# Kernel tuning notes

Measured on AMD Instinct MI355X. Metric: run time of the kernel, lower is better.

Reference implementation:

```python
import jax, jax.numpy as jnp
import numpy as np

BINS = 32
NUM_ACTION = 12


def _conv(x, w, b, stride, pad):
    y = jax.lax.conv_general_dilated(x, w, (stride, stride), [(pad, pad), (pad, pad)],
                                     dimension_numbers=('NCHW', 'OIHW', 'NCHW'))
    return y + b[None, :, None, None]


def _maxpool3s2(x):
    return jax.lax.reduce_window(x, -jnp.inf, jax.lax.max, (1, 1, 3, 3), (1, 1, 2, 2), 'VALID')


def _area_resize(x, oh, ow):
    b, c, h, w = x.shape  # exact area interp when h%oh==0, w%ow==0
    return x.reshape(b, c, oh, h // oh, ow, w // ow).mean(axis=(3, 5))


def _sobel_mag(gray):
    # kornia.filters.Sobel: normalized sobel kernels (abs-sum=1), replicate pad, sqrt(gx^2+gy^2+eps)
    kx = jnp.array([[-1., 0., 1.], [-2., 0., 2.], [-1., 0., 1.]], jnp.float32) / 8.0
    k = jnp.stack([kx, kx.T])[:, None]  # [2,1,3,3]
    p = jnp.pad(gray, ((0, 0), (0, 0), (1, 1), (1, 1)), mode='edge')
    g = jax.lax.conv_general_dilated(p, k, (1, 1), 'VALID',
                                     dimension_numbers=('NCHW', 'OIHW', 'NCHW'))
    return jnp.sqrt(jnp.sum(g * g, axis=1, keepdims=True) + 1e-6)


def _hist_feature(img):
    # Fused replacement for FeatureExtractor's python triple-loop of torch.histc calls.
    # img: [B,1,H,W] with values in [0,1]. Scale 0: whole-image hist; scale 1: the 4
    # quadrants of the full-res image; third bins-slot stays zero (loop only runs 2 scales).
    b, _, h, w = img.shape
    idx = jnp.clip((img[:, 0] * BINS).astype(jnp.int32), 0, BINS - 1)  # [B,H,W]
    hist = lambda i: jnp.zeros((BINS,), jnp.float32).at[i.ravel()].add(1.0)
    h0 = jax.vmap(hist)(idx) / (h * w)                                  # [B,BINS]
    h2, w2 = h // 2, w // 2
    blocks = idx.reshape(b, 2, h2, 2, w2).transpose(0, 1, 3, 2, 4).reshape(b * 4, h2 * w2)
    h1 = jax.vmap(hist)(blocks).reshape(b, 2, 2, BINS) / (h2 * w2)      # [B,2,2,BINS]
    out0 = jnp.broadcast_to(h0[:, :, None, None], (b, BINS, 4, 4))
    out1 = jnp.repeat(jnp.repeat(h1.transpose(0, 3, 1, 2), 2, axis=2), 2, axis=3)
    out2 = jnp.zeros_like(out0)
    return jnp.concatenate([out0, out1, out2], axis=1)                  # [B,3*BINS,4,4]


def _l2norm(x):
    return x / (jnp.linalg.norm(x, axis=1, keepdims=True) + 1e-7)


def _forward(image, w1, b1, w2, b2, w3, b3, w4, b4, w5, b5, fc1_w, fc1_b, fc2_w, fc2_b):
    b = image.shape[0]
    rgb = jnp.stack([image[:, 0], 0.5 * (image[:, 1] + image[:, 2]), image[:, 3]], axis=1)
    # AlexNet conv backbone on area-resized 112x112 -> [B,256,2,2]
    x = _area_resize(rgb, 112, 112)
    x = _maxpool3s2(jax.nn.relu(_conv(x, w1, b1, 4, 2)))
    x = _maxpool3s2(jax.nn.relu(_conv(x, w2, b2, 1, 2)))
    x = jax.nn.relu(_conv(x, w3, b3, 1, 1))
    x = jax.nn.relu(_conv(x, w4, b4, 1, 1))
    x = _maxpool3s2(jax.nn.relu(_conv(x, w5, b5, 1, 1)))
    f_sem = x.reshape(b, -1)                                            # [B,1024]
    gray = (0.299 * rgb[:, 0] + 0.587 * rgb[:, 1] + 0.114 * rgb[:, 2])[:, None]
    f_inten = _hist_feature(gray).reshape(b, -1)                        # [B,1536]
    f_grad = _hist_feature(_sobel_mag(gray)).reshape(b, -1)             # [B,1536]
    f_cat = jnp.concatenate([_l2norm(f_sem), _l2norm(f_inten), _l2norm(f_grad)], axis=1)
    h = jax.nn.relu(f_cat)                                              # Dropout = identity (eval)
    h = jax.nn.relu(h @ fc1_w.T + fc1_b)
    return h @ fc2_w.T + fc2_b                                          # [B,NUM_ACTION]


def setup_inputs() -> dict:
    key = jax.random.key(0)
    ks = jax.random.split(key, 8)
    B = 64
    image = jax.random.uniform(ks[0], (B, 4, 448, 448), jnp.float32)
    w = lambda k, shape, s=0.02: jax.random.normal(k, shape, jnp.float32) * s
    return {
        'image': image,
        'w1': w(ks[1], (64, 3, 11, 11)), 'b1': jnp.zeros((64,), jnp.float32),
        'w2': w(ks[2], (192, 64, 5, 5)), 'b2': jnp.zeros((192,), jnp.float32),
        'w3': w(ks[3], (384, 192, 3, 3)), 'b3': jnp.zeros((384,), jnp.float32),
        'w4': w(ks[4], (256, 384, 3, 3)), 'b4': jnp.zeros((256,), jnp.float32),
        'w5': w(ks[5], (256, 256, 3, 3)), 'b5': jnp.zeros((256,), jnp.float32),
        'fc1_w': w(ks[6], (256, 4096), 0.01), 'fc1_b': jnp.zeros((256,), jnp.float32),
        'fc2_w': w(ks[7], (NUM_ACTION, 256), 0.05), 'fc2_b': jnp.zeros((NUM_ACTION,), jnp.float32),
    }


def reference(image, w1, b1, w2, b2, w3, b3, w4, b4, w5, b5, fc1_w, fc1_b, fc2_w, fc2_b):
    return _forward(image, w1, b1, w2, b2, w3, b3, w4, b4, w5, b5, fc1_w, fc1_b, fc2_w, fc2_b)
```

## Files before the change

### kernel.cpp

```cpp
#include <hip/hip_runtime.h>
#include <math.h>

typedef __attribute__((ext_vector_type(8))) short short8;
typedef __attribute__((ext_vector_type(8))) unsigned short u16x8;
typedef __attribute__((ext_vector_type(4))) float f32x4;
typedef unsigned short ushort_t;

constexpr size_t OFF_HINT = 0;
constexpr size_t OFF_HGRD = OFF_HINT + (size_t)64*160;
constexpr size_t OFF_F    = OFF_HGRD + (size_t)64*160;
constexpr size_t OFF_H1   = OFF_F    + (size_t)64*4096;
constexpr size_t OFF_P5   = OFF_H1   + (size_t)64*256;
constexpr size_t OFF_WHI  = OFF_P5   + (size_t)64*1024;
constexpr size_t W1_OFF = 0;         constexpr int K1T = 363,  K1R = 384;
constexpr size_t W2_OFF = 24576;     constexpr int K2T = 1600, K2R = 1664;
constexpr size_t W3_OFF = 344064;    constexpr int K3T = 1728, K3R = 1792;
constexpr size_t W4_OFF = 1032192;   constexpr int K4T = 3456, K4R = 3456;
constexpr size_t W5_OFF = 1916928;   constexpr int K5T = 2304, K5R = 2304;
constexpr size_t WP_U16 = 2506752;
constexpr size_t OFF_WLO  = OFF_WHI + WP_U16/2;
constexpr size_t OFF_RA   = OFF_WLO + WP_U16/2;
constexpr size_t SZ_RA    = (size_t)2583552/2;
constexpr size_t A4P_U16  = 786432;
constexpr size_t OFF_RB   = OFF_RA + SZ_RA;
constexpr size_t SZ_RB    = (size_t)2985984/2;
constexpr size_t WS_FLOATS = OFF_RB + SZ_RB;

__device__ __forceinline__ void bf16split(float v, unsigned short& hi, unsigned short& lo) {
  union { float f; unsigned u; } a; a.f = v;
  unsigned uh = (a.u + 0x7FFFu + ((a.u >> 16) & 1u)) >> 16;
  hi = (unsigned short)uh;
  union { unsigned u; float f; } b; b.u = uh << 16;
  float rem = v - b.f;
  union { float f; unsigned u; } c; c.f = rem;
  lo = (unsigned short)((c.u + 0x7FFFu + ((c.u >> 16) & 1u)) >> 16);
}
__device__ __forceinline__ ushort_t f2bf(float f) {
  union { float f; unsigned u; } a; a.f = f;
  return (ushort_t)((a.u + 0x7FFFu + ((a.u >> 16) & 1u)) >> 16);
}
__device__ __forceinline__ float bf2f(ushort_t u) {
  union { unsigned u; float f; } a; a.u = ((unsigned)u) << 16; return a.f;
}

__global__ __launch_bounds__(256) void k_wsplit_all(const float* __restrict__ w1,
                                                    const float* __restrict__ w2,
                                                    const float* __restrict__ w3,
                                                    const float* __restrict__ w4,
                                                    const float* __restrict__ w5,
                                                    ushort_t* __restrict__ whi,
                                                    ushort_t* __restrict__ wlo) {
  const size_t idx = (size_t)blockIdx.x * 256 + threadIdx.x;
  if (idx >= WP_U16) return;
  const float* w; int kt, kr; size_t base;
  if (idx < W2_OFF)                { w = w1; kt = K1T; kr = K1R; base = W1_OFF; }
  else if (idx < W3_OFF)           { w = w2; kt = K2T; kr = K2R; base = W2_OFF; }
  else if (idx < W4_OFF)           { w = w3; kt = K3T; kr = K3R; base = W3_OFF; }
  else if (idx < W5_OFF)           { w = w4; kt = K4T; kr = K4R; base = W4_OFF; }
  else                             { w = w5; kt = K5T; kr = K5R; base = W5_OFF; }
  const size_t rel = idx - base;
  const int m = (int)(rel / kr), k = (int)(rel - (size_t)m * kr);
  const float v = (k < kt) ? w[(size_t)m * kt + k] : 0.f;
  unsigned short h, l;
  bf16split(v, h, l);
  whi[idx] = h; wlo[idx] = l;
}

__global__ __launch_bounds__(256) void k_preproc(const float* __restrict__ img,
                                                 float* __restrict__ hint,
                                                 float* __restrict__ hgrd,
                                                 ushort_t* __restrict__ x0) {
  const int b = blockIdx.x, s = blockIdx.y;
  const int r0 = s * 8;
  __shared__ float gs[10][448];
  __shared__ unsigned char lh[64 * 260];
  __shared__ ushort_t part[8 * 112 * 3];
  const int tid = threadIdx.x;
  for (int i = tid; i < (64 * 260) / 4; i += 256) ((unsigned*)lh)[i] = 0u;
  const float* ib = img + (size_t)b * 4 * 200704;
  for (int i = tid; i < 10 * 112; i += 256) {
    const int rr = i / 112, cc = i % 112, c4 = cc * 4;
    int r = r0 + rr - 1; r = r < 0 ? 0 : (r > 447 ? 447 : r);
    const size_t o = (size_t)r * 448 + c4;
    const float4 vr = *(const float4*)&ib[o];
    const float4 g1 = *(const float4*)&ib[200704 + o];
    const float4 g2 = *(const float4*)&ib[2 * 200704 + o];
    const float4 vb = *(const float4*)&ib[3 * 200704 + o];
    float4 g;
    g.x = 0.299f * vr.x + 0.587f * (0.5f * (g1.x + g2.x)) + 0.114f * vb.x;
    g.y = 0.299f * vr.y + 0.587f * (0.5f * (g1.y + g2.y)) + 0.114f * vb.y;
    g.z = 0.299f * vr.z + 0.587f * (0.5f * (g1.z + g2.z)) + 0.114f * vb.z;
    g.w = 0.299f * vr.w + 0.587f * (0.5f * (g1.w + g2.w)) + 0.114f * vb.w;
    *(float4*)&gs[rr][c4] = g;
    if (rr >= 1 && rr <= 8) {
      const float sr = vr.x + vr.y + vr.z + vr.w;
      const float sg = 0.5f * (g1.x + g2.x) + 0.5f * (g1.y + g2.y)
                     + 0.5f * (g1.z + g2.z) + 0.5f * (g1.w + g2.w);
      const float sb = vb.x + vb.y + vb.z + vb.w;
      ushort_t* pp = &part[((rr - 1) * 112 + cc) * 3];
      pp[0] = f2bf(sr); pp[1] = f2bf(sg); pp[2] = f2bf(sb);
    }
  }
  __syncthreads();
  for (int i = tid; i < 672; i += 256) {
    const int cc = i % 112;
    const int t  = i / 112;
    const int or2 = t & 1, ch = t >> 1;
    float sum = 0.f;
    #pragma unroll
    for (int rw = 0; rw < 4; ++rw)
      sum += bf2f(part[((or2 * 4 + rw) * 112 + cc) * 3 + ch]);
    x0[(((size_t)b * 3 + ch) * 116 + 2 + 2 * s + or2) * 116 + 2 + cc] = f2bf(sum * (1.f / 16.f));
  }
  for (int i = tid; i < 8 * 112; i += 256) {
    const int dr = i / 112, c4 = (i % 112) * 4;
    const unsigned colbit = (c4 >= 224) ? 1u : 0u;
    const float4 m1 = *(const float4*)&gs[dr + 1][c4];
    const float gv[4] = {m1.x, m1.y, m1.z, m1.w};
    #pragma unroll
    for (int j = 0; j < 4; ++j) {
      int bin = (int)(gv[j] * 32.f); bin = bin > 31 ? 31 : (bin < 0 ? 0 : bin);
      lh[(colbit * 32u + (unsigned)bin) * 260u + (unsigned)tid]++;
    }
  }
  __syncthreads();
  const unsigned rowbit = (s >= 28) ? 1u : 0u;
  {
    const int key = tid >> 2, quarter = tid & 3;
    const unsigned* row = (const unsigned*)&lh[(unsigned)key * 260u];
    unsigned sum = 0;
    #pragma unroll
    for (int d = 0; d < 16; ++d) {
      const unsigned v = row[quarter * 16 + d];
      sum += (v & 0xFFu) + ((v >> 8) & 0xFFu) + ((v >> 16) & 0xFFu) + (v >> 24);
    }
    sum += __shfl_down(sum, 1, 64);
    sum += __shfl_down(sum, 2, 64);
    if (quarter == 0) {
      const int colbit2 = key >> 5, bin = key & 31;
      atomicAdd(&hint[(size_t)b * 160 + 32 + (rowbit * 2 + colbit2) * 32 + bin], (float)sum);
    }
  }
  __syncthreads();
  for (int i = tid; i < (64 * 260) / 4; i += 256) ((unsigned*)lh)[i] = 0u;
  __syncthreads();
  for (int i = tid; i < 8 * 112; i += 256) {
    const int dr = i / 112, c4 = (i % 112) * 4;
    const unsigned colbit = (c4 >= 224) ? 1u : 0u;
    const int cl = c4 > 0 ? c4 - 1 : 0;
    const int cr = c4 < 444 ? c4 + 4 : 447;
    const float4 m0 = *(const float4*)&gs[dr][c4];
    const float4 m1 = *(const float4*)&gs[dr + 1][c4];
    const float4 m2 = *(const float4*)&gs[dr + 2][c4];
    const float r0v[6] = {gs[dr][cl],     m0.x, m0.y, m0.z, m0.w, gs[dr][cr]};
    const float r1v[6] = {gs[dr + 1][cl], m1.x, m1.y, m1.z, m1.w, gs[dr + 1][cr]};
    const float r2v[6] = {gs[dr + 2][cl], m2.x, m2.y, m2.z, m2.w, gs[dr + 2][cr]};
    #pragma unroll
    for (int j = 0; j < 4; ++j) {
      const float gx = (-r0v[j] + r0v[j + 2] - 2.f * r1v[j] + 2.f * r1v[j + 2]
                        - r2v[j] + r2v[j + 2]) * 0.125f;
      const float gy = (-r0v[j] - 2.f * r0v[j + 1] - r0v[j + 2]
                        + r2v[j] + 2.f * r2v[j + 1] + r2v[j + 2]) * 0.125f;
      const float mag = sqrtf(gx * gx + gy * gy + 1e-6f);
      int sb = (int)(mag * 32.f); sb = sb > 31 ? 31 : (sb < 0 ? 0 : sb);
      lh[(colbit * 32u + (unsigned)sb) * 260u + (unsigned)tid]++;
    }
  }
  __syncthreads();
  {
    const int key = tid >> 2, quarter = tid & 3;
    const unsigned* row = (const unsigned*)&lh[(unsigned)key * 260u];
    unsigned sum = 0;
    #pragma unroll
    for (int d = 0; d < 16; ++d) {
      const unsigned v = row[quarter * 16 + d];
      sum += (v & 0xFFu) + ((v >> 8) & 0xFFu) + ((v >> 16) & 0xFFu) + (v >> 24);
    }
    sum += __shfl_down(sum, 1, 64);
    sum += __shfl_down(sum, 2, 64);
    if (quarter == 0) {
      const int colbit2 = key >> 5, bin = key & 31;
      atomicAdd(&hgrd[(size_t)b * 160 + 32 + (rowbit * 2 + colbit2) * 32 + bin], (float)sum);
    }
  }
}

template<int CIN, int HP, int WP, int KH, int KW, int STRIDE, int OH, int OW,
         int OHP, int OWP, int OPAD, int M, int MT>
__global__ __launch_bounds__(512) void k_conv_mfma(const ushort_t* __restrict__ in,
                                                   const ushort_t* __restrict__ whi_,
                                                   const ushort_t* __restrict__ wlo_,
                                                   const float* __restrict__ bias,
                                                   ushort_t* __restrict__ out) {
  constexpr int K_TOT  = CIN * KH * KW;
  constexpr int K_ROUND = ((K_TOT + 127) / 128) * 128;
  constexpr int GSTEPS = K_ROUND / 128;
  constexpr int KHW = KH * KW;
  constexpr int NPB = OH * OW;
  constexpr int WROWS = MT / 16;
  constexpr int TGRP  = 4 / WROWS;
  constexpr int TFRAG = 4 / TGRP;
  __shared__ ushort_t Bs[2][2][64 * 64];
  __shared__ ushort_t ftab[K_ROUND];
  const int tid = threadIdx.x;
  const int lane = tid & 63, wv = tid >> 6;
  const int g = wv >> 2, wg = wv & 3;
  const int sub = tid & 255;
  const int n0 = blockIdx.x * 64, m0 = blockIdx.y * MT;
  for (int k = tid; k < K_ROUND; k += 512) {
    const int c = k / KHW, kr = k - c * KHW;
    const int ky = kr / KW, kx = kr - (kr / KW) * KW;
    ftab[k] = (k < K_TOT) ? (ushort_t)(2 * ((c * HP + ky) * WP + kx)) : (ushort_t)0;
  }
  const int col = sub & 63, kc2 = sub >> 6;
  const int nb = n0 + col;
  const int bB = nb / NPB, rB = nb % NPB;
  const int oyB = rB / OW, oxB = rB % OW;
  const char* baseB = (const char*)(in + (size_t)bB * CIN * HP * WP)
                      + 2 * (oyB * STRIDE * WP + oxB * STRIDE);
  const int wm = wg % WROWS, tg = wg / WROWS;
  const int mrow = m0 + wm * 16 + (lane & 15);
  const ushort_t* wh = whi_ + (size_t)mrow * K_ROUND;
  const ushort_t* wl = wlo_ + (size_t)mrow * K_ROUND;
  const int kA = (lane >> 4) * 8;
  f32x4 acc[TFRAG] = {};
  const int kb0 = g * GSTEPS * 64;
  __syncthreads();

  u16x8 rb0, rb1;
  short8 rah0, ral0, rah1, ral1;
  {
    const int kb = kb0;
    const u16x8 f0 = *(const u16x8*)&ftab[kb + kc2 * 16];
    const u16x8 f1 = *(const u16x8*)&ftab[kb + kc2 * 16 + 8];
    #pragma unroll
    for (int j = 0; j < 8; ++j) rb0[j] = *(const ushort_t*)(baseB + f0[j]);
    #pragma unroll
    for (int j = 0; j < 8; ++j) rb1[j] = *(const ushort_t*)(baseB + f1[j]);
    rah0 = *(const short8*)&wh[kb + kA];
    ral0 = *(const short8*)&wl[kb + kA];
    rah1 = *(const short8*)&wh[kb + 32 + kA];
    ral1 = *(const short8*)&wl[kb + 32 + kA];
  }
  {
    const int c0 = kc2 * 2, c1 = c0 + 1;
    *(u16x8*)&Bs[g][0][col * 64 + ((c0 ^ (col & 7)) * 8)] = rb0;
    *(u16x8*)&Bs[g][0][col * 64 + ((c1 ^ (col & 7)) * 8)] = rb1;
  }
  __syncthreads();
  int cur = 0;
  for (int step = 0; step < GSTEPS; ++step) {
    const short8 a_h0 = rah0, a_l0 = ral0, a_h1 = rah1, a_l1 = ral1;
    if (step + 1 < GSTEPS) {
      const int kb = kb0 + (step + 1) * 64;
      const u16x8 f0 = *(const u16x8*)&ftab[kb + kc2 * 16];
      const u16x8 f1 = *(const u16x8*)&ftab[kb + kc2 * 16 + 8];
      #pragma unroll
      for (int j = 0; j < 8; ++j) rb0[j] = *(const ushort_t*)(baseB + f0[j]);
      #pragma unroll
      for (int j = 0; j < 8; ++j) rb1[j] = *(const ushort_t*)(baseB + f1[j]);
      rah0 = *(const short8*)&wh[kb + kA];
      ral0 = *(const short8*)&wl[kb + kA];
      rah1 = *(const short8*)&wh[kb + 32 + kA];
      ral1 = *(const short8*)&wl[kb + 32 + kA];
    }
    #pragma unroll
    for (int s = 0; s < 2; ++s) {
      const short8 a_h = s ? a_h1 : a_h0;
      const short8 a_l = s ? a_l1 : a_l0;
      const int cA = s * 4 + (lane >> 4);
      #pragma unroll
      for (int tt = 0; tt < TFRAG; ++tt) {
        const int t = tg * TFRAG + tt;
        const int coln = t * 16 + (lane & 15);
        const short8 b_v = *(const short8*)&Bs[g][cur][coln * 64 + ((cA ^ (coln & 7)) * 8)];
        acc[tt] = __builtin_amdgcn_mfma_f32_16x16x32_bf16(a_h, b_v, acc[tt], 0, 0, 0);
        acc[tt] = __builtin_amdgcn_mfma_f32_16x16x32_bf16(a_l, b_v, acc[tt], 0, 0, 0);
      }
    }
    if (step + 1 < GSTEPS) {
      const int c0 = kc2 * 2, c1 = c0 + 1;
      *(u16x8*)&Bs[g][cur ^ 1][col * 64 + ((c0 ^ (col & 7)) * 8)] = rb0;
      *(u16x8*)&Bs[g][cur ^ 1][col * 64 + ((c1 ^ (col & 7)) * 8)] = rb1;
      __syncthreads();
      cur ^= 1;
    }
  }
  __syncthreads();
  float* scratch = (float*)&Bs[0][0][0];
  if (g == 1) {
    #pragma unroll
    for (int tt = 0; tt < TFRAG; ++tt) {
      const int t = tg * TFRAG + tt;
      #pragma unroll
      for (int q = 0; q < 4; ++q)
        scratch[(wm * 16 + (lane >> 4) * 4 + q) * 64 + t * 16 + (lane & 15)] = acc[tt][q];
    }
  }
  __syncthreads();
  if (g == 0) {
    #pragma unroll
    for (int q = 0; q < 4; ++q) {
      const int m = m0 + wm * 16 + (lane >> 4) * 4 + q;
      const float bi = bias[m];
      #pragma unroll
      for (int tt = 0; tt < TFRAG; ++tt) {
        const int t = tg * TFRAG + tt;
        const int n = n0 + t * 16 + (lane & 15);
        const float v = acc[tt][q]
                      + scratch[(wm * 16 + (lane >> 4) * 4 + q) * 64 + t * 16 + (lane & 15)]
                      + bi;
        const int b = n / NPB, r = n % NPB;
        const int oy = r / OW, ox = r - (r / OW) * OW;
        out[(((size_t)b * M + m) * OHP + OPAD + oy) * OWP + OPAD + ox] = f2bf(fmaxf(v, 0.f));
      }
    }
  }
}

template<int C, int HI, int HO, int HOP, int PAD, bool OUTF32>
__global__ __launch_bounds__(256) void k_pool(const ushort_t* __restrict__ in,
                                              void* __restrict__ out) {
  const int idx = blockIdx.x * 256 + threadIdx.x;
  constexpr int TOT = 64 * C * HOP * HOP;
  if (idx >= TOT) return;
  const int x = idx % HOP;
  const int y = (idx / HOP) % HOP;
  const int c = (idx / (HOP * HOP)) % C;
  const int b = idx / (HOP * HOP * C);
  ushort_t v = 0;
  const int oy = y - PAD, ox = x - PAD;
  if (oy >= 0 && oy < HO && ox >= 0 && ox < HO) {
    const ushort_t* ib = in + (size_t)(b * C + c) * HI * HI + (size_t)(oy * 2) * HI + ox * 2;
    #pragma unroll
    for (int i = 0; i < 3; ++i)
      #pragma unroll
      for (int j = 0; j < 3; ++j) {
        const ushort_t u = ib[i * HI + j];
        v = u > v ? u : v;
      }
  }
  if constexpr (OUTF32) ((float*)out)[idx] = bf2f(v);
  else                  ((ushort_t*)out)[idx] = v;
}

__global__ __launch_bounds__(256) void k_feat(const float* __restrict__ p5,
                                              const float* __restrict__ hint,
                                              const float* __restrict__ hgrad,
                                              float* __restrict__ f) {
  const int b = blockIdx.x, tid = threadIdx.x;
  __shared__ float tmp4[4];
  __shared__ float vals[160];
  const float* ps = p5 + (size_t)b * 1024;
  float* fb = f + (size_t)b * 4096;
  float mv[4]; float ss = 0.f;
  #pragma unroll
  for (int i = 0; i < 4; ++i) { mv[i] = ps[tid + i * 256]; ss += mv[i] * mv[i]; }
  #pragma unroll
  for (int o = 32; o > 0; o >>= 1) ss += __shfl_down(ss, o, 64);
  if ((tid & 63) == 0) tmp4[tid >> 6] = ss;
  __syncthreads();
  const float inv = 1.f / (sqrtf(tmp4[0] + tmp4[1] + tmp4[2] + tmp4[3]) + 1e-7f);
  #pragma unroll
  for (int i = 0; i < 4; ++i) fb[tid + i * 256] = fmaxf(mv[i] * inv, 0.f);
  for (int ft = 0; ft < 2; ++ft) {
    const float* hb = (ft ? hgrad : hint) + (size_t)b * 160;
    __syncthreads();
    if (tid < 160) {
      float cnt;
      if (tid < 32) cnt = hb[32 + tid] + hb[64 + tid] + hb[96 + tid] + hb[128 + tid];
      else          cnt = hb[tid];
      vals[tid] = cnt * (tid < 32 ? (1.f / 200704.f) : (1.f / 50176.f));
    }
    __syncthreads();
    float s2 = 0.f;
    if (tid < 160) s2 = (tid < 32 ? 16.f : 4.f) * vals[tid] * vals[tid];
    #pragma unroll
    for (int o = 32; o > 0; o >>= 1) s2 += __shfl_down(s2, o, 64);
    __syncthreads();
    if ((tid & 63) == 0) tmp4[tid >> 6] = s2;
    __syncthreads();
    const float inv2 = 1.f / (sqrtf(tmp4[0] + tmp4[1] + tmp4[2] + tmp4[3]) + 1e-7f);
    float* fo = fb + 1024 + ft * 1536;
    for (int idx = tid; idx < 1536; idx += 256) {
      const int ch = idx >> 4, i2 = (idx >> 2) & 3, j = idx & 3;
      float v;
      if (ch < 32)      v = vals[ch];
      else if (ch < 64) v = vals[32 + (((i2 >> 1) * 2) + (j >> 1)) * 32 + (ch - 32)];
      else              v = 0.f;
      fo[idx] = fmaxf(v * inv2, 0.f);
    }
  }
}

__global__ __launch_bounds__(256) void k_fc1(const float* __restrict__ f,
                                             const float* __restrict__ w,
                                             const float* __restrict__ bias,
                                             float* __restrict__ h1) {
  const int gid = blockIdx.x * 4 + (threadIdx.x >> 6);
  const int lane = threadIdx.x & 63;
  if (gid >= 256 * 8) return;
  const int oc = gid >> 3, bg = gid & 7;
  const float* wr = w + (size_t)oc * 4096;
  const float* fb = f + (size_t)(bg * 8) * 4096;
  float s[8] = {};
  for (int k = lane; k < 4096; k += 64) {
    const float wv = wr[k];
    #pragma unroll
    for (int i = 0; i < 8; ++i) s[i] += wv * fb[(size_t)i * 4096 + k];
  }
  #pragma unroll
  for (int i = 0; i < 8; ++i) {
    #pragma unroll
    for (int o = 32; o > 0; o >>= 1) s[i] += __shfl_down(s[i], o, 64);
  }
  if (lane == 0) {
    const float bi = bias[oc];
    #pragma unroll
    for (int i = 0; i < 8; ++i)
      h1[(size_t)(bg * 8 + i) * 256 + oc] = fmaxf(s[i] + bi, 0.f);
  }
}

__global__ __launch_bounds__(256) void k_fc2_simple(const float* __restrict__ h1,
                                                    const float* __restrict__ w,
                                                    const float* __restrict__ bias,
                                                    float* __restrict__ out) {
  const int idx = blockIdx.x * 256 + threadIdx.x;
  if (idx >= 64 * 12) return;
  const int oc = idx % 12, b = idx / 12;
  const float* hb = h1 + (size_t)b * 256;
  const float* wr = w + (size_t)oc * 256;
  float s = bias[oc];
  for (int k = 0; k < 256; ++k) s += hb[k] * wr[k];
  out[b * 12 + oc] = s;
}

extern "C" void kernel_launch(void* const* d_in, const int* in_sizes, int n_in,
                              void* d_out, int out_size, void* d_ws, size_t ws_size,
                              hipStream_t stream) {
  const float* img  = (const float*)d_in[0];
  const float* w1 = (const float*)d_in[1];  const float* b1 = (const float*)d_in[2];
  const float* w2 = (const float*)d_in[3];  const float* b2 = (const float*)d_in[4];
  const float* w3 = (const float*)d_in[5];  const float* b3 = (const float*)d_in[6];
  const float* w4 = (const float*)d_in[7];  const float* b4 = (const float*)d_in[8];
  const float* w5 = (const float*)d_in[9];  const float* b5 = (const float*)d_in[10];
  const float* fc1w = (const float*)d_in[11]; const float* fc1b = (const float*)d_in[12];
  const float* fc2w = (const float*)d_in[13]; const float* fc2b = (const float*)d_in[14];
  float* out = (float*)d_out;
  float* ws  = (float*)d_ws;

  float* hint = ws + OFF_HINT;
  float* hgrd = ws + OFF_HGRD;
  float* f    = ws + OFF_F;
  float* h1   = ws + OFF_H1;
  float* p5   = ws + OFF_P5;
  ushort_t* whi = (ushort_t*)(ws + OFF_WHI);
  ushort_t* wlo = (ushort_t*)(ws + OFF_WLO);
  ushort_t* ra  = (ushort_t*)(ws + OFF_RA);
  ushort_t* rb  = (ushort_t*)(ws + OFF_RB);

  hipMemsetAsync(hint, 0, (size_t)2 * 64 * 160 * sizeof(float), stream);
  hipMemsetAsync(ra, 0, (size_t)64 * 3 * 116 * 116 * 2, stream);

  k_wsplit_all<<<(int)((WP_U16 + 255) / 256), 256, 0, stream>>>(w1, w2, w3, w4, w5, whi, wlo);

  k_preproc<<<dim3(64, 56), 256, 0, stream>>>(img, hint, hgrd, ra);

  k_conv_mfma<3,116,116,11,11,4,27,27,27,27,0,64,64>
      <<<dim3(729, 1), 512, 0, stream>>>(ra, whi + W1_OFF, wlo + W1_OFF, b1, rb);
  k_pool<64,27,13,17,2,false><<<(64*64*17*17 + 255)/256, 256, 0, stream>>>(rb, ra);
  k_conv_mfma<64,17,17,5,5,1,13,13,13,13,0,192,64>
      <<<dim3(169, 3), 512, 0, stream>>>(ra, whi + W2_OFF, wlo + W2_OFF, b2, rb);
  k_pool<192,13,6,8,1,false><<<(64*192*8*8 + 255)/256, 256, 0, stream>>>(rb, ra);
  hipMemsetAsync(rb, 0, (size_t)64*384*8*8*2, stream);
  hipMemsetAsync(ra + A4P_U16, 0, (size_t)64*256*8*8*2, stream);
  k_conv_mfma<192,8,8,3,3,1,6,6,8,8,1,384,32>
      <<<dim3(36, 12), 512, 0, stream>>>(ra, whi + W3_OFF, wlo + W3_OFF, b3, rb);
  k_conv_mfma<384,8,8,3,3,1,6,6,8,8,1,256,32>
      <<<dim3(36, 8), 512, 0, stream>>>(rb, whi + W4_OFF, wlo + W4_OFF, b4, ra + A4P_U16);
  k_conv_mfma<256,8,8,3,3,1,6,6,6,6,0,256,32>
      <<<dim3(36, 8), 512, 0, stream>>>(ra + A4P_U16, whi + W5_OFF, wlo + W5_OFF, b5, rb);
  k_pool<256,6,2,2,0,true><<<(64*256*2*2 + 255)/256, 256, 0, stream>>>(rb, p5);

  k_feat<<<64, 256, 0, stream>>>(p5, hint, hgrd, f);
  k_fc1<<<(256*8)/4, 256, 0, stream>>>(f, fc1w, fc1b, h1);
  k_fc2_simple<<<(64*12 + 255)/256, 256, 0, stream>>>(h1, fc2w, fc2b, out);
}
```

Measured before the change: 448.9 us.

## Switch conv activations to NHWC layout with vectorized channel-contiguous loads

Converts the activation tensors from NCHW to NHWC and reorders the packed weight K dimension to (ky,kx,c). For layers where CIN is a multiple of 16, the conv B-operand gather becomes two 16-byte vector loads instead of sixteen scalar 2-byte loads, and the epilogue writes four output channels as one packed store. The pool kernels are re-indexed for the new layout, and the final pool converts back to NCHW for the feature stage. Conv1 (CIN=3) still uses the scalar gather, and the strided channel access in pooling may reduce coalescing there.

```diff
diff --git a/kernel.cpp b/kernel.cpp
--- a/kernel.cpp
+++ b/kernel.cpp
@@ -3,6 +3,7 @@
 
 typedef __attribute__((ext_vector_type(8))) short short8;
 typedef __attribute__((ext_vector_type(8))) unsigned short u16x8;
+typedef __attribute__((ext_vector_type(4))) unsigned short u16x4;
 typedef __attribute__((ext_vector_type(4))) float f32x4;
 typedef unsigned short ushort_t;
 
@@ -52,15 +53,19 @@
                                                     ushort_t* __restrict__ wlo) {
   const size_t idx = (size_t)blockIdx.x * 256 + threadIdx.x;
   if (idx >= WP_U16) return;
-  const float* w; int kt, kr; size_t base;
-  if (idx < W2_OFF)                { w = w1; kt = K1T; kr = K1R; base = W1_OFF; }
-  else if (idx < W3_OFF)           { w = w2; kt = K2T; kr = K2R; base = W2_OFF; }
-  else if (idx < W4_OFF)           { w = w3; kt = K3T; kr = K3R; base = W3_OFF; }
-  else if (idx < W5_OFF)           { w = w4; kt = K4T; kr = K4R; base = W4_OFF; }
-  else                             { w = w5; kt = K5T; kr = K5R; base = W5_OFF; }
+  const float* w; int cin, khw, kt, kr; size_t base;
+  if (idx < W2_OFF)      { w = w1; cin = 3;   khw = 121; kt = K1T; kr = K1R; base = W1_OFF; }
+  else if (idx < W3_OFF) { w = w2; cin = 64;  khw = 25;  kt = K2T; kr = K2R; base = W2_OFF; }
+  else if (idx < W4_OFF) { w = w3; cin = 192; khw = 9;   kt = K3T; kr = K3R; base = W3_OFF; }
+  else if (idx < W5_OFF) { w = w4; cin = 384; khw = 9;   kt = K4T; kr = K4R; base = W4_OFF; }
+  else                   { w = w5; cin = 256; khw = 9;   kt = K5T; kr = K5R; base = W5_OFF; }
   const size_t rel = idx - base;
   const int m = (int)(rel / kr), k = (int)(rel - (size_t)m * kr);
-  const float v = (k < kt) ? w[(size_t)m * kt + k] : 0.f;
+  float v = 0.f;
+  if (k < kt) {
+    const int kyx = k / cin, c = k - kyx * cin;
+    v = w[(size_t)m * kt + c * khw + kyx];
+  }
   unsigned short h, l;
   bf16split(v, h, l);
   whi[idx] = h; wlo[idx] = l;
@@ -110,7 +115,8 @@
     #pragma unroll
     for (int rw = 0; rw < 4; ++rw)
       sum += bf2f(part[((or2 * 4 + rw) * 112 + cc) * 3 + ch]);
-    x0[(((size_t)b * 3 + ch) * 116 + 2 + 2 * s + or2) * 116 + 2 + cc] = f2bf(sum * (1.f / 16.f));
+    x0[(((size_t)b * 116 + (2 + 2 * s + or2)) * 116 + (2 + cc)) * 3 + ch]
+        = f2bf(sum * (1.f / 16.f));
   }
   for (int i = tid; i < 8 * 112; i += 256) {
     const int dr = i / 112, c4 = (i % 112) * 4;
@@ -195,7 +201,6 @@
   constexpr int K_TOT  = CIN * KH * KW;
   constexpr int K_ROUND = ((K_TOT + 127) / 128) * 128;
   constexpr int GSTEPS = K_ROUND / 128;
-  constexpr int KHW = KH * KW;
   constexpr int NPB = OH * OW;
   constexpr int WROWS = MT / 16;
   constexpr int TGRP  = 4 / WROWS;
@@ -208,16 +213,16 @@
   const int sub = tid & 255;
   const int n0 = blockIdx.x * 64, m0 = blockIdx.y * MT;
   for (int k = tid; k < K_ROUND; k += 512) {
-    const int c = k / KHW, kr = k - c * KHW;
-    const int ky = kr / KW, kx = kr - (kr / KW) * KW;
-    ftab[k] = (k < K_TOT) ? (ushort_t)(2 * ((c * HP + ky) * WP + kx)) : (ushort_t)0;
+    const int kyx = k / CIN, c = k - kyx * CIN;
+    const int ky = kyx / KW, kx = kyx - (kyx / KW) * KW;
+    ftab[k] = (k < K_TOT) ? (ushort_t)(2 * ((ky * WP + kx) * CIN + c)) : (ushort_t)0;
   }
   const int col = sub & 63, kc2 = sub >> 6;
   const int nb = n0 + col;
   const int bB = nb / NPB, rB = nb % NPB;
   const int oyB = rB / OW, oxB = rB % OW;
-  const char* baseB = (const char*)(in + (size_t)bB * CIN * HP * WP)
-                      + 2 * (oyB * STRIDE * WP + oxB * STRIDE);
+  const char* baseB = (const char*)(in + (size_t)bB * HP * WP * CIN)
+                      + 2 * (size_t)(oyB * STRIDE * WP + oxB * STRIDE) * CIN;
   const int wm = wg % WROWS, tg = wg / WROWS;
   const int mrow = m0 + wm * 16 + (lane & 15);
   const ushort_t* wh = whi_ + (size_t)mrow * K_ROUND;
@@ -229,36 +234,40 @@
 
   u16x8 rb0, rb1;
   short8 rah0, ral0, rah1, ral1;
-  {
-    const int kb = kb0;
-    const u16x8 f0 = *(const u16x8*)&ftab[kb + kc2 * 16];
-    const u16x8 f1 = *(const u16x8*)&ftab[kb + kc2 * 16 + 8];
-    #pragma unroll
-    for (int j = 0; j < 8; ++j) rb0[j] = *(const ushort_t*)(baseB + f0[j]);
-    #pragma unroll
-    for (int j = 0; j < 8; ++j) rb1[j] = *(const ushort_t*)(baseB + f1[j]);
-    rah0 = *(const short8*)&wh[kb + kA];
-    ral0 = *(const short8*)&wl[kb + kA];
-    rah1 = *(const short8*)&wh[kb + 32 + kA];
-    ral1 = *(const short8*)&wl[kb + 32 + kA];
-  }
-  {
-    const int c0 = kc2 * 2, c1 = c0 + 1;
-    *(u16x8*)&Bs[g][0][col * 64 + ((c0 ^ (col & 7)) * 8)] = rb0;
-    *(u16x8*)&Bs[g][0][col * 64 + ((c1 ^ (col & 7)) * 8)] = rb1;
-  }
-  __syncthreads();
-  int cur = 0;
-  for (int step = 0; step < GSTEPS; ++step) {
-    const short8 a_h0 = rah0, a_l0 = ral0, a_h1 = rah1, a_l1 = ral1;
-    if (step + 1 < GSTEPS) {
-      const int kb = kb0 + (step + 1) * 64;
+  auto loadB = [&](int kb) {
+    if constexpr (CIN % 16 == 0) {
+      const char* p = baseB + ftab[kb + kc2 * 16];
+      rb0 = *(const u16x8*)(p);
+      rb1 = *(const u16x8*)(p + 16);
+    } else {
       const u16x8 f0 = *(const u16x8*)&ftab[kb + kc2 * 16];
       const u16x8 f1 = *(const u16x8*)&ftab[kb + kc2 * 16 + 8];
       #pragma unroll
       for (int j = 0; j < 8; ++j) rb0[j] = *(const ushort_t*)(baseB + f0[j]);
       #pragma unroll
       for (int j = 0; j < 8; ++j) rb1[j] = *(const ushort_t*)(baseB + f1[j]);
+    }
+  };
+  {
+    const int kb = kb0;
+    loadB(kb);
+    rah0 = *(const short8*)&wh[kb + kA];
+    ral0 = *(const short8*)&wl[kb + kA];
+    rah1 = *(const short8*)&wh[kb + 32 + kA];
+    ral1 = *(const short8*)&wl[kb + 32 + kA];
+  }
+  {
+    const int c0 = kc2 * 2, c1 = c0 + 1;
+    *(u16x8*)&Bs[g][0][col * 64 + ((c0 ^ (col & 7)) * 8)] = rb0;
+    *(u16x8*)&Bs[g][0][col * 64 + ((c1 ^ (col & 7)) * 8)] = rb1;
+  }
+  __syncthreads();
+  int cur = 0;
+  for (int step = 0; step < GSTEPS; ++step) {
+    const short8 a_h0 = rah0, a_l0 = ral0, a_h1 = rah1, a_l1 = ral1;
+    if (step + 1 < GSTEPS) {
+      const int kb = kb0 + (step + 1) * 64;
+      loadB(kb);
       rah0 = *(const short8*)&wh[kb + kA];
       ral0 = *(const short8*)&wl[kb + kA];
       rah1 = *(const short8*)&wh[kb + 32 + kA];
@@ -299,21 +308,23 @@
   }
   __syncthreads();
   if (g == 0) {
-    #pragma unroll
-    for (int q = 0; q < 4; ++q) {
-      const int m = m0 + wm * 16 + (lane >> 4) * 4 + q;
-      const float bi = bias[m];
+    const int mb = m0 + wm * 16 + (lane >> 4) * 4;
+    #pragma unroll
+    for (int tt = 0; tt < TFRAG; ++tt) {
+      const int t = tg * TFRAG + tt;
+      const int nl = t * 16 + (lane & 15);
+      const int n = n0 + nl;
+      const int b = n / NPB, r = n % NPB;
+      const int oy = r / OW, ox = r - (r / OW) * OW;
+      u16x4 pk;
       #pragma unroll
-      for (int tt = 0; tt < TFRAG; ++tt) {
-        const int t = tg * TFRAG + tt;
-        const int n = n0 + t * 16 + (lane & 15);
+      for (int q = 0; q < 4; ++q) {
         const float v = acc[tt][q]
-                      + scratch[(wm * 16 + (lane >> 4) * 4 + q) * 64 + t * 16 + (lane & 15)]
-                      + bi;
-        const int b = n / NPB, r = n % NPB;
-        const int oy = r / OW, ox = r - (r / OW) * OW;
-        out[(((size_t)b * M + m) * OHP + OPAD + oy) * OWP + OPAD + ox] = f2bf(fmaxf(v, 0.f));
+                      + scratch[(wm * 16 + (lane >> 4) * 4 + q) * 64 + nl]
+                      + bias[mb + q];
+        pk[q] = f2bf(fmaxf(v, 0.f));
       }
+      *(u16x4*)&out[(((size_t)b * OHP + OPAD + oy) * OWP + (OPAD + ox)) * M + mb] = pk;
     }
   }
 }
@@ -324,24 +335,26 @@
   const int idx = blockIdx.x * 256 + threadIdx.x;
   constexpr int TOT = 64 * C * HOP * HOP;
   if (idx >= TOT) return;
-  const int x = idx % HOP;
-  const int y = (idx / HOP) % HOP;
-  const int c = (idx / (HOP * HOP)) % C;
-  const int b = idx / (HOP * HOP * C);
+  const int c = idx % C;
+  const int x = (idx / C) % HOP;
+  const int y = (idx / (C * HOP)) % HOP;
+  const int b = idx / (C * HOP * HOP);
   ushort_t v = 0;
   const int oy = y - PAD, ox = x - PAD;
   if (oy >= 0 && oy < HO && ox >= 0 && ox < HO) {
-    const ushort_t* ib = in + (size_t)(b * C + c) * HI * HI + (size_t)(oy * 2) * HI + ox * 2;
+    const ushort_t* ib = in + (((size_t)b * HI + oy * 2) * HI + ox * 2) * C + c;
     #pragma unroll
     for (int i = 0; i < 3; ++i)
       #pragma unroll
       for (int j = 0; j < 3; ++j) {
-        const ushort_t u = ib[i * HI + j];
+        const ushort_t u = ib[(i * HI + j) * C];
         v = u > v ? u : v;
       }
   }
-  if constexpr (OUTF32) ((float*)out)[idx] = bf2f(v);
-  else                  ((ushort_t*)out)[idx] = v;
+  if constexpr (OUTF32)
+    ((float*)out)[((size_t)b * C + c) * (HO * HO) + y * HO + x] = bf2f(v);
+  else
+    ((ushort_t*)out)[idx] = v;
 }
 
 __global__ __launch_bounds__(256) void k_feat(const float* __restrict__ p5,
@@ -461,7 +474,7 @@
   ushort_t* rb  = (ushort_t*)(ws + OFF_RB);
 
   hipMemsetAsync(hint, 0, (size_t)2 * 64 * 160 * sizeof(float), stream);
-  hipMemsetAsync(ra, 0, (size_t)64 * 3 * 116 * 116 * 2, stream);
+  hipMemsetAsync(ra, 0, (size_t)64 * 116 * 116 * 3 * 2, stream);
 
   k_wsplit_all<<<(int)((WP_U16 + 255) / 256), 256, 0, stream>>>(w1, w2, w3, w4, w5, whi, wlo);
 
```

After: 374.4 us. -16.6%, faster.
